# Kernel tuning notes

Hardware: AMD Instinct MI355X
Metric: run time of the kernel (lower is better)

Reference implementation:

```python
import jax, jax.numpy as jnp
import numpy as np

DIM = 2048
N_HEADS = 32
N_KV_HEADS = 8
HEAD_DIM = DIM // N_HEADS  # 64
GROUP = N_HEADS // N_KV_HEADS  # 4
ROPE_BASE = 10000.0


def setup_inputs() -> dict:
    key = jax.random.key(0)
    k1, k2, k3, k4, k5 = jax.random.split(key, 5)
    b, s = 1, 2048
    scale = 1.0 / np.sqrt(DIM)
    return {
        "x": jax.random.normal(k1, (b, s, DIM), dtype=jnp.float32),
        # weights stored as (in, out); equivalent math to torch Linear (x @ W.T)
        "wq": jax.random.normal(k2, (DIM, N_HEADS * HEAD_DIM), dtype=jnp.float32) * scale,
        "wk": jax.random.normal(k3, (DIM, N_KV_HEADS * HEAD_DIM), dtype=jnp.float32) * scale,
        "wv": jax.random.normal(k4, (DIM, N_KV_HEADS * HEAD_DIM), dtype=jnp.float32) * scale,
        "wo": jax.random.normal(k5, (N_HEADS * HEAD_DIM, DIM), dtype=jnp.float32) * scale,
    }


def _rope_cos_sin(seq_len, dtype):
    inv_freq = 1.0 / (ROPE_BASE ** (jnp.arange(0, HEAD_DIM, 2, dtype=jnp.float32) / HEAD_DIM))
    t = jnp.arange(seq_len, dtype=jnp.float32)
    freqs = jnp.outer(t, inv_freq)              # [s, hd/2]
    emb = jnp.concatenate([freqs, freqs], -1)   # [s, hd]
    return jnp.cos(emb).astype(dtype), jnp.sin(emb).astype(dtype)


def _rotate_half(x):
    x1, x2 = x[..., : HEAD_DIM // 2], x[..., HEAD_DIM // 2 :]
    return jnp.concatenate([-x2, x1], axis=-1)


def reference(x, wq, wk, wv, wo):
    b, s, _ = x.shape
    q = (x @ wq).reshape(b, s, N_HEADS, HEAD_DIM)
    k = (x @ wk).reshape(b, s, N_KV_HEADS, HEAD_DIM)
    v = (x @ wv).reshape(b, s, N_KV_HEADS, HEAD_DIM)

    cos, sin = _rope_cos_sin(s, x.dtype)
    cos = cos[None, :, None, :]  # [1, s, 1, hd] broadcast over batch & heads
    sin = sin[None, :, None, :]
    q = q * cos + _rotate_half(q) * sin
    k = k * cos + _rotate_half(k) * sin

    # GQA: repeat KV heads (repeat_interleave along head dim)
    k = jnp.repeat(k, GROUP, axis=2)  # [b, s, n_heads, hd]
    v = jnp.repeat(v, GROUP, axis=2)

    q = q.transpose(0, 2, 1, 3)  # [b, h, s, d]
    k = k.transpose(0, 2, 1, 3)
    v = v.transpose(0, 2, 1, 3)

    scores = jnp.einsum("bhqd,bhkd->bhqk", q, k) / jnp.sqrt(jnp.asarray(HEAD_DIM, x.dtype))
    attn = jax.nn.softmax(scores, axis=-1)
    out = jnp.einsum("bhqk,bhkd->bhqd", attn, v)
    out = out.transpose(0, 2, 1, 3).reshape(b, s, N_HEADS * HEAD_DIM)
    return out @ wo
```

## Files before the change

kernel.cpp:

```cpp
#include <hip/hip_runtime.h>
#include <hip/hip_bf16.h>

typedef __bf16 bf16x8 __attribute__((ext_vector_type(8)));
typedef __bf16 bf16x4 __attribute__((ext_vector_type(4)));
typedef float fx4 __attribute__((ext_vector_type(4)));
typedef float fx16 __attribute__((ext_vector_type(16)));

#define AS1 __attribute__((address_space(1)))
#define AS3 __attribute__((address_space(3)))

__global__ __launch_bounds__(256) void cast_x(const float4* __restrict__ X, __bf16* __restrict__ Xb) {
    int i = blockIdx.x * 256 + threadIdx.x;
    float4 v = X[i];
    bf16x4 o = { (__bf16)v.x, (__bf16)v.y, (__bf16)v.z, (__bf16)v.w };
    *(bf16x4*)(Xb + (size_t)i * 4) = o;
}

__global__ __launch_bounds__(256) void transpose_all(const float* __restrict__ wq, const float* __restrict__ wk,
                                                     const float* __restrict__ wv, const float* __restrict__ wo,
                                                     __bf16* __restrict__ WqkvT, __bf16* __restrict__ WoT) {
    constexpr int K = 2048;
    __shared__ float t[32][33];
    const int bx = blockIdx.x;
    const float* W; __bf16* Wt; int N, n0;
    if (bx < 64)      { W = wq; Wt = WqkvT;                        N = 2048; n0 = bx * 32; }
    else if (bx < 80) { W = wk; Wt = WqkvT + (size_t)2048 * 2048;  N = 512;  n0 = (bx - 64) * 32; }
    else if (bx < 96) { W = wv; Wt = WqkvT + (size_t)2560 * 2048;  N = 512;  n0 = (bx - 80) * 32; }
    else              { W = wo; Wt = WoT;                          N = 2048; n0 = (bx - 96) * 32; }
    const int tx = threadIdx.x & 31, ty = threadIdx.x >> 5;
    const int k0 = blockIdx.y * 32;
#pragma unroll
    for (int i = 0; i < 4; ++i)
        t[ty + i * 8][tx] = W[(size_t)(k0 + ty + i * 8) * N + n0 + tx];
    __syncthreads();
#pragma unroll
    for (int i = 0; i < 4; ++i)
        Wt[(size_t)(n0 + ty + i * 8) * K + k0 + tx] = (__bf16)t[tx][ty + i * 8];
}

__global__ __launch_bounds__(256) void gemm_qkv(const __bf16* __restrict__ A, const __bf16* __restrict__ Bt,
                                                __bf16* __restrict__ Qr, __bf16* __restrict__ Kr,
                                                __bf16* __restrict__ Vt) {
    constexpr int K = 2048;
    __shared__ __align__(16) __bf16 lA[2][128 * 32];
    __shared__ __align__(16) __bf16 lB[2][64 * 32];
    const int tid = threadIdx.x;
    const int wave = tid >> 6, lane = tid & 63;
    const int quad = lane >> 4, l16 = lane & 15;
    const int m0 = blockIdx.x * 128, n0 = blockIdx.y * 64;
    fx4 acc[2][4] = {};

    const __bf16* csrc[6]; __bf16* cdst[6];
#pragma unroll
    for (int it = 0; it < 6; ++it) {
        const int idx = wave * 6 + it;
        const int r4 = lane >> 2, c8 = (lane & 3) * 8;
        if (idx < 16) {
            const int kh = idx & 1, s = idx >> 1;
            csrc[it] = A + (size_t)(m0 + s * 16 + r4) * K + kh * 32 + c8;
            cdst[it] = &lA[kh][s * 512 + lane * 8];
        } else {
            const int b = idx - 16, kh = b & 1, s = b >> 1;
            csrc[it] = Bt + (size_t)(n0 + s * 16 + r4) * K + kh * 32 + c8;
            cdst[it] = &lB[kh][s * 512 + lane * 8];
        }
    }

    for (int k0 = 0; k0 < K; k0 += 64) {
        __syncthreads();
#pragma unroll
        for (int it = 0; it < 6; ++it)
            __builtin_amdgcn_global_load_lds((const AS1 void*)(csrc[it] + k0),
                                             (AS3 void*)cdst[it], 16, 0, 0);
        __builtin_amdgcn_s_waitcnt(0);
        __syncthreads();

#pragma unroll
        for (int kc = 0; kc < 2; ++kc) {
            bf16x8 af[2], bfr[4];
#pragma unroll
            for (int i = 0; i < 2; ++i) af[i] = *(const bf16x8*)&lA[kc][(wave * 32 + i * 16 + l16) * 32 + quad * 8];
#pragma unroll
            for (int j = 0; j < 4; ++j) bfr[j] = *(const bf16x8*)&lB[kc][(j * 16 + l16) * 32 + quad * 8];
#pragma unroll
            for (int i = 0; i < 2; ++i)
#pragma unroll
                for (int j = 0; j < 4; ++j)
                    acc[i][j] = __builtin_amdgcn_mfma_f32_16x16x32_bf16(af[i], bfr[j], acc[i][j], 0, 0, 0);
        }
    }

    const int by = blockIdx.y;
    if (by < 40) {
        const float scale = (by < 32) ? 0.18033688011112042f : 1.0f;
        __bf16* base = (by < 32) ? (Qr + (size_t)by * 2048 * 64)
                                 : (Kr + (size_t)(by - 32) * 2048 * 64);
#pragma unroll
        for (int jj = 0; jj < 2; ++jj) {
            const int dlo = jj * 16 + l16;
            const float inv = __builtin_amdgcn_exp2f(-(float)dlo * 0.41524101186092029f);
#pragma unroll
            for (int i = 0; i < 2; ++i)
#pragma unroll
                for (int r = 0; r < 4; ++r) {
                    const int s = m0 + wave * 32 + i * 16 + quad * 4 + r;
                    float sn, cs;
                    __sincosf((float)s * inv, &sn, &cs);
                    const float lo = acc[i][jj][r], hv = acc[i][jj + 2][r];
                    base[(size_t)s * 64 + dlo]      = (__bf16)((lo * cs - hv * sn) * scale);
                    base[(size_t)s * 64 + dlo + 32] = (__bf16)((hv * cs + lo * sn) * scale);
                }
        }
    } else {
        __bf16* vb = Vt + (size_t)(by - 40) * 64 * 2048;
#pragma unroll
        for (int i = 0; i < 2; ++i)
#pragma unroll
            for (int j = 0; j < 4; ++j) {
                const int d = j * 16 + l16;
                const int s0 = m0 + wave * 32 + i * 16 + quad * 4;
                bf16x4 p;
#pragma unroll
                for (int r = 0; r < 4; ++r) p[r] = (__bf16)acc[i][j][r];
                *(bf16x4*)&vb[(size_t)d * 2048 + s0] = p;
            }
    }
}

__global__ __launch_bounds__(256) void gemm_bt_sk(const __bf16* __restrict__ A, const __bf16* __restrict__ Bt,
                                                  float* __restrict__ C0, float* __restrict__ C1,
                                                  int M, int N, int K) {
    __shared__ __align__(16) __bf16 lA[128 * 32];
    __shared__ __align__(16) __bf16 lB[128 * 32];
    const int tid = threadIdx.x;
    const int wave = tid >> 6, lane = tid & 63;
    const int quad = lane >> 4, l16 = lane & 15;
    const int m0 = blockIdx.x * 128, n0 = blockIdx.y * 128;
    const int kz = blockIdx.z;
    const int kbeg = kz * (K >> 1), kend = kbeg + (K >> 1);
    float* C = kz ? C1 : C0;
    const int wm = (wave >> 1) * 64, wn = (wave & 1) * 64;
    fx4 acc[4][4] = {};

    const int st0 = wave * 1024;
    const int st1 = 4096 + wave * 1024;
    const int r0 = (st0 + lane * 16) >> 6, c0 = ((st0 + lane * 16) & 63) >> 1;
    const int r1 = (st1 + lane * 16) >> 6, c1 = ((st1 + lane * 16) & 63) >> 1;

    for (int k0 = kbeg; k0 < kend; k0 += 32) {
        __syncthreads();
        __builtin_amdgcn_global_load_lds((const AS1 void*)(A + (size_t)(m0 + r0) * K + k0 + c0),
                                         (AS3 void*)(lA + (st0 >> 1)), 16, 0, 0);
        __builtin_amdgcn_global_load_lds((const AS1 void*)(A + (size_t)(m0 + r1) * K + k0 + c1),
                                         (AS3 void*)(lA + (st1 >> 1)), 16, 0, 0);
        __builtin_amdgcn_global_load_lds((const AS1 void*)(Bt + (size_t)(n0 + r0) * K + k0 + c0),
                                         (AS3 void*)(lB + (st0 >> 1)), 16, 0, 0);
        __builtin_amdgcn_global_load_lds((const AS1 void*)(Bt + (size_t)(n0 + r1) * K + k0 + c1),
                                         (AS3 void*)(lB + (st1 >> 1)), 16, 0, 0);
        __builtin_amdgcn_s_waitcnt(0);
        __syncthreads();

        bf16x8 af[4], bfr[4];
#pragma unroll
        for (int i = 0; i < 4; ++i) af[i] = *(const bf16x8*)&lA[(wm + i * 16 + l16) * 32 + quad * 8];
#pragma unroll
        for (int j = 0; j < 4; ++j) bfr[j] = *(const bf16x8*)&lB[(wn + j * 16 + l16) * 32 + quad * 8];
#pragma unroll
        for (int i = 0; i < 4; ++i)
#pragma unroll
            for (int j = 0; j < 4; ++j)
                acc[i][j] = __builtin_amdgcn_mfma_f32_16x16x32_bf16(af[i], bfr[j], acc[i][j], 0, 0, 0);
    }
#pragma unroll
    for (int i = 0; i < 4; ++i)
#pragma unroll
        for (int j = 0; j < 4; ++j) {
            const int row = m0 + wm + i * 16 + quad * 4;
            const int col = n0 + wn + j * 16 + l16;
#pragma unroll
            for (int r = 0; r < 4; ++r)
                C[(size_t)(row + r) * N + col] = acc[i][j][r];
        }
}

__global__ __launch_bounds__(256) void reduce_add(float4* __restrict__ out, const float4* __restrict__ p) {
    const int i = blockIdx.x * 256 + threadIdx.x;
    float4 a = out[i];
    const float4 b = p[i];
    a.x += b.x; a.y += b.y; a.z += b.z; a.w += b.w;
    out[i] = a;
}

__global__ __launch_bounds__(512, 4) void flash_attn(const __bf16* __restrict__ Qr, const __bf16* __restrict__ Kr,
                                                     const __bf16* __restrict__ Vt, __bf16* __restrict__ O) {
    constexpr int S = 2048;
    __shared__ __align__(16) __bf16 smem[2][4 * 64 * 72];
    const int qt = blockIdx.x, h = blockIdx.y, kvh = h >> 2;
    const int tid = threadIdx.x, wave = tid >> 6, lane = tid & 63;
    const int grp = wave >> 2, w4 = wave & 3;
    const int l32 = lane & 31, hi = lane >> 5;
    const int goff = grp * 2 * 4608;

    const int qrow = qt * 128 + w4 * 32 + l32;
    const __bf16* qptr = Qr + ((size_t)h * S + qrow) * 64;
    bf16x8 qf[4];
#pragma unroll
    for (int kc = 0; kc < 4; ++kc) qf[kc] = *(const bf16x8*)(qptr + kc * 16 + hi * 8);

    const __bf16* Kbase = Kr + (size_t)kvh * S * 64;
    const __bf16* Vbase = Vt + (size_t)kvh * 64 * S;

    const int gtid = tid & 255;
    const int krow = gtid >> 3;
    const int kcol = (gtid & 7) * 8;
    const int vslot = (kcol & 48) | ((kcol & 8) >> 1);

    bf16x8 kreg0 = *(const bf16x8*)(Kbase + (size_t)(grp * 64 + krow) * 64 + kcol);
    bf16x8 kreg1 = *(const bf16x8*)(Kbase + (size_t)(grp * 64 + 32 + krow) * 64 + kcol);
    bf16x8 vreg0 = *(const bf16x8*)(Vbase + (size_t)krow * S + grp * 64 + kcol);
    bf16x8 vreg1 = *(const bf16x8*)(Vbase + (size_t)(32 + krow) * S + grp * 64 + kcol);

    fx16 ov0, ov1;
#pragma unroll
    for (int i = 0; i < 16; ++i) { ov0[i] = 0.f; ov1[i] = 0.f; }
    float l_acc = 0.f;

    {
        __bf16* nK = &smem[0][goff];
        __bf16* nV = nK + 4608;
        *(bf16x8*)&nK[krow * 72 + kcol] = kreg0;
        *(bf16x8*)&nK[(32 + krow) * 72 + kcol] = kreg1;
        bf16x4 v0lo = { vreg0[0], vreg0[1], vreg0[2], vreg0[3] };
        bf16x4 v0hi = { vreg0[4], vreg0[5], vreg0[6], vreg0[7] };
        bf16x4 v1lo = { vreg1[0], vreg1[1], vreg1[2], vreg1[3] };
        bf16x4 v1hi = { vreg1[4], vreg1[5], vreg1[6], vreg1[7] };
        *(bf16x4*)&nV[krow * 72 + vslot]            = v0lo;
        *(bf16x4*)&nV[krow * 72 + vslot + 8]        = v0hi;
        *(bf16x4*)&nV[(32 + krow) * 72 + vslot]     = v1lo;
        *(bf16x4*)&nV[(32 + krow) * 72 + vslot + 8] = v1hi;
        const int kt1 = 2 + grp;
        kreg0 = *(const bf16x8*)(Kbase + (size_t)(kt1 * 64 + krow) * 64 + kcol);
        kreg1 = *(const bf16x8*)(Kbase + (size_t)(kt1 * 64 + 32 + krow) * 64 + kcol);
        vreg0 = *(const bf16x8*)(Vbase + (size_t)krow * S + kt1 * 64 + kcol);
        vreg1 = *(const bf16x8*)(Vbase + (size_t)(32 + krow) * S + kt1 * 64 + kcol);
    }
    __syncthreads();

    for (int it = 0; it < 16; ++it) {
        __bf16* lKg = &smem[it & 1][goff];
        __bf16* lVg = lKg + 4608;

        if (it + 1 < 16) {
            __bf16* nK = &smem[(it + 1) & 1][goff];
            __bf16* nV = nK + 4608;
            *(bf16x8*)&nK[krow * 72 + kcol] = kreg0;
            *(bf16x8*)&nK[(32 + krow) * 72 + kcol] = kreg1;
            bf16x4 v0lo = { vreg0[0], vreg0[1], vreg0[2], vreg0[3] };
            bf16x4 v0hi = { vreg0[4], vreg0[5], vreg0[6], vreg0[7] };
            bf16x4 v1lo = { vreg1[0], vreg1[1], vreg1[2], vreg1[3] };
            bf16x4 v1hi = { vreg1[4], vreg1[5], vreg1[6], vreg1[7] };
            *(bf16x4*)&nV[krow * 72 + vslot]            = v0lo;
            *(bf16x4*)&nV[krow * 72 + vslot + 8]        = v0hi;
            *(bf16x4*)&nV[(32 + krow) * 72 + vslot]     = v1lo;
            *(bf16x4*)&nV[(32 + krow) * 72 + vslot + 8] = v1hi;
            const int it2 = (it + 2 < 16) ? it + 2 : 15;
            const int ktn = it2 * 2 + grp;
            kreg0 = *(const bf16x8*)(Kbase + (size_t)(ktn * 64 + krow) * 64 + kcol);
            kreg1 = *(const bf16x8*)(Kbase + (size_t)(ktn * 64 + 32 + krow) * 64 + kcol);
            vreg0 = *(const bf16x8*)(Vbase + (size_t)krow * S + ktn * 64 + kcol);
            vreg1 = *(const bf16x8*)(Vbase + (size_t)(32 + krow) * S + ktn * 64 + kcol);
        }

        fx16 sc0, sc1;
#pragma unroll
        for (int i = 0; i < 16; ++i) { sc0[i] = 0.f; sc1[i] = 0.f; }
#pragma unroll
        for (int kc = 0; kc < 4; ++kc) {
            const bf16x8 a0 = *(const bf16x8*)&lKg[l32 * 72 + kc * 16 + hi * 8];
            const bf16x8 a1 = *(const bf16x8*)&lKg[(32 + l32) * 72 + kc * 16 + hi * 8];
            sc0 = __builtin_amdgcn_mfma_f32_32x32x16_bf16(a0, qf[kc], sc0, 0, 0, 0);
            sc1 = __builtin_amdgcn_mfma_f32_32x32x16_bf16(a1, qf[kc], sc1, 0, 0, 0);
        }

#pragma unroll
        for (int h2 = 0; h2 < 2; ++h2) {
#pragma unroll
            for (int c = 0; c < 2; ++c) {
                bf16x8 pb;
#pragma unroll
                for (int j = 0; j < 8; ++j) {
                    const float sv = h2 ? sc1[c * 8 + j] : sc0[c * 8 + j];
                    const float p = __builtin_amdgcn_exp2f(sv);
                    l_acc += p;
                    pb[j] = (__bf16)p;
                }
                const int kcv = h2 * 2 + c;
                const bf16x8 va0 = *(const bf16x8*)&lVg[l32 * 72 + kcv * 16 + hi * 8];
                const bf16x8 va1 = *(const bf16x8*)&lVg[(32 + l32) * 72 + kcv * 16 + hi * 8];
                ov0 = __builtin_amdgcn_mfma_f32_32x32x16_bf16(va0, pb, ov0, 0, 0, 0);
                ov1 = __builtin_amdgcn_mfma_f32_32x32x16_bf16(va1, pb, ov1, 0, 0, 0);
            }
        }
        __syncthreads();
    }

    const float l_pair = l_acc + __shfl_xor(l_acc, 32, 64);

    fx4* lO = (fx4*)&smem[0][0];
    float* lL = (float*)(&smem[0][0] + 16384);
    if (grp == 1) {
#pragma unroll
        for (int ic = 0; ic < 4; ++ic) {
            fx4 c0, c1;
#pragma unroll
            for (int r = 0; r < 4; ++r) { c0[r] = ov0[ic * 4 + r]; c1[r] = ov1[ic * 4 + r]; }
            lO[(ic * 4 + w4) * 64 + lane] = c0;
            lO[((ic + 4) * 4 + w4) * 64 + lane] = c1;
        }
        if (hi == 0) lL[w4 * 32 + l32] = l_pair;
    }
    __syncthreads();
    if (grp == 0) {
#pragma unroll
        for (int ic = 0; ic < 4; ++ic) {
            const fx4 c0 = lO[(ic * 4 + w4) * 64 + lane];
            const fx4 c1 = lO[((ic + 4) * 4 + w4) * 64 + lane];
#pragma unroll
            for (int r = 0; r < 4; ++r) { ov0[ic * 4 + r] += c0[r]; ov1[ic * 4 + r] += c1[r]; }
        }
        const float inv_l = 1.0f / (l_pair + lL[w4 * 32 + l32]);
#pragma unroll
        for (int dt = 0; dt < 2; ++dt)
#pragma unroll
            for (int rg2 = 0; rg2 < 4; ++rg2) {
                bf16x4 o4;
#pragma unroll
                for (int r = 0; r < 4; ++r)
                    o4[r] = (__bf16)((dt ? ov1[rg2 * 4 + r] : ov0[rg2 * 4 + r]) * inv_l);
                const int col = h * 64 + dt * 32 + rg2 * 8 + hi * 4;
                *(bf16x4*)(O + (size_t)qrow * 2048 + col) = o4;
            }
    }
}

extern "C" void kernel_launch(void* const* d_in, const int* in_sizes, int n_in,
                              void* d_out, int out_size, void* d_ws, size_t ws_size,
                              hipStream_t stream) {
    const float* x  = (const float*)d_in[0];
    const float* wq = (const float*)d_in[1];
    const float* wk = (const float*)d_in[2];
    const float* wv = (const float*)d_in[3];
    const float* wo = (const float*)d_in[4];
    float* out = (float*)d_out;
    char* ws = (char*)d_ws;

    __bf16* Xb    = (__bf16*)ws;
    __bf16* WqkvT = (__bf16*)(ws + ((size_t)8 << 20));
    __bf16* WoT   = (__bf16*)(ws + ((size_t)20 << 20));
    __bf16* Qr    = (__bf16*)(ws + ((size_t)28 << 20));
    __bf16* Kr    = (__bf16*)(ws + ((size_t)36 << 20));
    __bf16* Vt    = (__bf16*)(ws + ((size_t)38 << 20));
    __bf16* Ob    = (__bf16*)(ws + ((size_t)40 << 20));
    float*  Cp    = (float*)ws;

    cast_x<<<4096, 256, 0, stream>>>((const float4*)x, Xb);
    transpose_all<<<dim3(160, 64), 256, 0, stream>>>(wq, wk, wv, wo, WqkvT, WoT);

    gemm_qkv<<<dim3(16, 48), 256, 0, stream>>>(Xb, WqkvT, Qr, Kr, Vt);
    flash_attn<<<dim3(16, 32), 512, 0, stream>>>(Qr, Kr, Vt, Ob);
    gemm_bt_sk<<<dim3(16, 16, 2), 256, 0, stream>>>(Ob, WoT, out, Cp, 2048, 2048, 2048);
    reduce_add<<<4096, 256, 0, stream>>>((float4*)out, (const float4*)Cp);
}
```

Baseline: 222.1 us.

## Fuse prep kernels and double-buffer GEMM loads with XOR-swizzled LDS

Merges the x cast and the weight transpose into one launch, with larger transpose tiles and paired bf16 stores. Both GEMMs now use a double-buffered LDS pipeline that prefetches the next K-slice while MFMAs run on the current one, cutting the barrier count. LDS column offsets are XOR-swizzled to reduce bank conflicts. The cost is more LDS per block and more complex indexing.

```diff
diff --git a/kernel.cpp b/kernel.cpp
--- a/kernel.cpp
+++ b/kernel.cpp
@@ -3,91 +3,105 @@
 
 typedef __bf16 bf16x8 __attribute__((ext_vector_type(8)));
 typedef __bf16 bf16x4 __attribute__((ext_vector_type(4)));
+typedef __bf16 bf16x2 __attribute__((ext_vector_type(2)));
 typedef float fx4 __attribute__((ext_vector_type(4)));
 typedef float fx16 __attribute__((ext_vector_type(16)));
 
 #define AS1 __attribute__((address_space(1)))
 #define AS3 __attribute__((address_space(3)))
 
-__global__ __launch_bounds__(256) void cast_x(const float4* __restrict__ X, __bf16* __restrict__ Xb) {
-    int i = blockIdx.x * 256 + threadIdx.x;
-    float4 v = X[i];
-    bf16x4 o = { (__bf16)v.x, (__bf16)v.y, (__bf16)v.z, (__bf16)v.w };
-    *(bf16x4*)(Xb + (size_t)i * 4) = o;
-}
-
-__global__ __launch_bounds__(256) void transpose_all(const float* __restrict__ wq, const float* __restrict__ wk,
-                                                     const float* __restrict__ wv, const float* __restrict__ wo,
-                                                     __bf16* __restrict__ WqkvT, __bf16* __restrict__ WoT) {
+__global__ __launch_bounds__(256) void prep(const float4* __restrict__ X, __bf16* __restrict__ Xb,
+                                            const float* __restrict__ wq, const float* __restrict__ wk,
+                                            const float* __restrict__ wv, const float* __restrict__ wo,
+                                            __bf16* __restrict__ WqkvT, __bf16* __restrict__ WoT) {
+    const int bx = blockIdx.x;
+    if (bx < 4096) {
+        const int i = bx * 256 + threadIdx.x;
+        const float4 v = X[i];
+        bf16x4 o = { (__bf16)v.x, (__bf16)v.y, (__bf16)v.z, (__bf16)v.w };
+        *(bf16x4*)(Xb + (size_t)i * 4) = o;
+        return;
+    }
     constexpr int K = 2048;
-    __shared__ float t[32][33];
-    const int bx = blockIdx.x;
-    const float* W; __bf16* Wt; int N, n0;
-    if (bx < 64)      { W = wq; Wt = WqkvT;                        N = 2048; n0 = bx * 32; }
-    else if (bx < 80) { W = wk; Wt = WqkvT + (size_t)2048 * 2048;  N = 512;  n0 = (bx - 64) * 32; }
-    else if (bx < 96) { W = wv; Wt = WqkvT + (size_t)2560 * 2048;  N = 512;  n0 = (bx - 80) * 32; }
-    else              { W = wo; Wt = WoT;                          N = 2048; n0 = (bx - 96) * 32; }
+    __shared__ float t[64][33];
+    const int tt = bx - 4096;
+    const float* W; __bf16* Wt; int N, loc;
+    if (tt < 2048)      { W = wq; Wt = WqkvT;                       N = 2048; loc = tt; }
+    else if (tt < 2560) { W = wk; Wt = WqkvT + (size_t)2048 * 2048; N = 512;  loc = tt - 2048; }
+    else if (tt < 3072) { W = wv; Wt = WqkvT + (size_t)2560 * 2048; N = 512;  loc = tt - 2560; }
+    else                { W = wo; Wt = WoT;                         N = 2048; loc = tt - 3072; }
+    const int k0 = (loc & 31) * 64, n0 = (loc >> 5) * 32;
     const int tx = threadIdx.x & 31, ty = threadIdx.x >> 5;
-    const int k0 = blockIdx.y * 32;
-#pragma unroll
-    for (int i = 0; i < 4; ++i)
+#pragma unroll
+    for (int i = 0; i < 8; ++i)
         t[ty + i * 8][tx] = W[(size_t)(k0 + ty + i * 8) * N + n0 + tx];
     __syncthreads();
 #pragma unroll
-    for (int i = 0; i < 4; ++i)
-        Wt[(size_t)(n0 + ty + i * 8) * K + k0 + tx] = (__bf16)t[tx][ty + i * 8];
+    for (int i = 0; i < 4; ++i) {
+        const int nn = ty + i * 8;
+        bf16x2 o = { (__bf16)t[tx * 2][nn], (__bf16)t[tx * 2 + 1][nn] };
+        *(bf16x2*)&Wt[(size_t)(n0 + nn) * K + k0 + tx * 2] = o;
+    }
 }
 
 __global__ __launch_bounds__(256) void gemm_qkv(const __bf16* __restrict__ A, const __bf16* __restrict__ Bt,
                                                 __bf16* __restrict__ Qr, __bf16* __restrict__ Kr,
                                                 __bf16* __restrict__ Vt) {
     constexpr int K = 2048;
-    __shared__ __align__(16) __bf16 lA[2][128 * 32];
-    __shared__ __align__(16) __bf16 lB[2][64 * 32];
+    constexpr int BUF = 192 * 32;
+    __shared__ __align__(16) __bf16 sm[2][BUF];
     const int tid = threadIdx.x;
     const int wave = tid >> 6, lane = tid & 63;
     const int quad = lane >> 4, l16 = lane & 15;
     const int m0 = blockIdx.x * 128, n0 = blockIdx.y * 64;
     fx4 acc[2][4] = {};
 
-    const __bf16* csrc[6]; __bf16* cdst[6];
-#pragma unroll
-    for (int it = 0; it < 6; ++it) {
-        const int idx = wave * 6 + it;
-        const int r4 = lane >> 2, c8 = (lane & 3) * 8;
-        if (idx < 16) {
-            const int kh = idx & 1, s = idx >> 1;
-            csrc[it] = A + (size_t)(m0 + s * 16 + r4) * K + kh * 32 + c8;
-            cdst[it] = &lA[kh][s * 512 + lane * 8];
+    const int r4 = lane >> 2;
+    const int c8s = ((lane & 3) ^ ((r4 >> 1) & 3)) * 8;
+    const __bf16* csrc[3]; int cdst[3];
+#pragma unroll
+    for (int it = 0; it < 3; ++it) {
+        const int idx = wave * 3 + it;
+        if (idx < 8) {
+            csrc[it] = A + (size_t)(m0 + idx * 16 + r4) * K + c8s;
+            cdst[it] = idx * 512 + lane * 8;
         } else {
-            const int b = idx - 16, kh = b & 1, s = b >> 1;
-            csrc[it] = Bt + (size_t)(n0 + s * 16 + r4) * K + kh * 32 + c8;
-            cdst[it] = &lB[kh][s * 512 + lane * 8];
-        }
-    }
-
-    for (int k0 = 0; k0 < K; k0 += 64) {
-        __syncthreads();
-#pragma unroll
-        for (int it = 0; it < 6; ++it)
-            __builtin_amdgcn_global_load_lds((const AS1 void*)(csrc[it] + k0),
-                                             (AS3 void*)cdst[it], 16, 0, 0);
-        __builtin_amdgcn_s_waitcnt(0);
-        __syncthreads();
-
-#pragma unroll
-        for (int kc = 0; kc < 2; ++kc) {
-            bf16x8 af[2], bfr[4];
-#pragma unroll
-            for (int i = 0; i < 2; ++i) af[i] = *(const bf16x8*)&lA[kc][(wave * 32 + i * 16 + l16) * 32 + quad * 8];
-#pragma unroll
-            for (int j = 0; j < 4; ++j) bfr[j] = *(const bf16x8*)&lB[kc][(j * 16 + l16) * 32 + quad * 8];
-#pragma unroll
-            for (int i = 0; i < 2; ++i)
-#pragma unroll
-                for (int j = 0; j < 4; ++j)
-                    acc[i][j] = __builtin_amdgcn_mfma_f32_16x16x32_bf16(af[i], bfr[j], acc[i][j], 0, 0, 0);
-        }
+            const int s = idx - 8;
+            csrc[it] = Bt + (size_t)(n0 + s * 16 + r4) * K + c8s;
+            cdst[it] = 4096 + s * 512 + lane * 8;
+        }
+    }
+    const int colr = (quad ^ ((l16 >> 1) & 3)) * 8;
+    const int arow = (wave * 32 + l16) * 32 + colr;
+    const int brow = 4096 + l16 * 32 + colr;
+
+#pragma unroll
+    for (int it = 0; it < 3; ++it)
+        __builtin_amdgcn_global_load_lds((const AS1 void*)csrc[it], (AS3 void*)&sm[0][cdst[it]], 16, 0, 0);
+    __builtin_amdgcn_s_waitcnt(0);
+    __syncthreads();
+
+#pragma unroll 2
+    for (int t = 0; t < 64; ++t) {
+        if (t < 63) {
+            const int kofs = (t + 1) * 32;
+#pragma unroll
+            for (int it = 0; it < 3; ++it)
+                __builtin_amdgcn_global_load_lds((const AS1 void*)(csrc[it] + kofs),
+                                                 (AS3 void*)&sm[(t + 1) & 1][cdst[it]], 16, 0, 0);
+        }
+        const __bf16* cb = sm[t & 1];
+        bf16x8 af[2], bfr[4];
+#pragma unroll
+        for (int i = 0; i < 2; ++i) af[i] = *(const bf16x8*)&cb[arow + i * 512];
+#pragma unroll
+        for (int j = 0; j < 4; ++j) bfr[j] = *(const bf16x8*)&cb[brow + j * 512];
+#pragma unroll
+        for (int i = 0; i < 2; ++i)
+#pragma unroll
+            for (int j = 0; j < 4; ++j)
+                acc[i][j] = __builtin_amdgcn_mfma_f32_16x16x32_bf16(af[i], bfr[j], acc[i][j], 0, 0, 0);
+        if (t < 63) { __builtin_amdgcn_s_waitcnt(0); __syncthreads(); }
     }
 
     const int by = blockIdx.y;
@@ -129,47 +143,66 @@
 
 __global__ __launch_bounds__(256) void gemm_bt_sk(const __bf16* __restrict__ A, const __bf16* __restrict__ Bt,
                                                   float* __restrict__ C0, float* __restrict__ C1,
-                                                  int M, int N, int K) {
-    __shared__ __align__(16) __bf16 lA[128 * 32];
-    __shared__ __align__(16) __bf16 lB[128 * 32];
+                                                  int M, int N, int Kdim) {
+    constexpr int K = 2048;
+    constexpr int BUF = 256 * 32;
+    __shared__ __align__(16) __bf16 sm[2][BUF];
     const int tid = threadIdx.x;
     const int wave = tid >> 6, lane = tid & 63;
     const int quad = lane >> 4, l16 = lane & 15;
     const int m0 = blockIdx.x * 128, n0 = blockIdx.y * 128;
     const int kz = blockIdx.z;
-    const int kbeg = kz * (K >> 1), kend = kbeg + (K >> 1);
     float* C = kz ? C1 : C0;
     const int wm = (wave >> 1) * 64, wn = (wave & 1) * 64;
     fx4 acc[4][4] = {};
 
-    const int st0 = wave * 1024;
-    const int st1 = 4096 + wave * 1024;
-    const int r0 = (st0 + lane * 16) >> 6, c0 = ((st0 + lane * 16) & 63) >> 1;
-    const int r1 = (st1 + lane * 16) >> 6, c1 = ((st1 + lane * 16) & 63) >> 1;
-
-    for (int k0 = kbeg; k0 < kend; k0 += 32) {
-        __syncthreads();
-        __builtin_amdgcn_global_load_lds((const AS1 void*)(A + (size_t)(m0 + r0) * K + k0 + c0),
-                                         (AS3 void*)(lA + (st0 >> 1)), 16, 0, 0);
-        __builtin_amdgcn_global_load_lds((const AS1 void*)(A + (size_t)(m0 + r1) * K + k0 + c1),
-                                         (AS3 void*)(lA + (st1 >> 1)), 16, 0, 0);
-        __builtin_amdgcn_global_load_lds((const AS1 void*)(Bt + (size_t)(n0 + r0) * K + k0 + c0),
-                                         (AS3 void*)(lB + (st0 >> 1)), 16, 0, 0);
-        __builtin_amdgcn_global_load_lds((const AS1 void*)(Bt + (size_t)(n0 + r1) * K + k0 + c1),
-                                         (AS3 void*)(lB + (st1 >> 1)), 16, 0, 0);
-        __builtin_amdgcn_s_waitcnt(0);
-        __syncthreads();
-
+    const int r4 = lane >> 2;
+    const int c8s = ((lane & 3) ^ ((r4 >> 1) & 3)) * 8;
+    const __bf16* csrc[4]; int cdst[4];
+#pragma unroll
+    for (int it = 0; it < 4; ++it) {
+        const int idx = wave * 4 + it;
+        if (idx < 8) {
+            csrc[it] = A + (size_t)(m0 + idx * 16 + r4) * K + c8s;
+            cdst[it] = idx * 512 + lane * 8;
+        } else {
+            const int s = idx - 8;
+            csrc[it] = Bt + (size_t)(n0 + s * 16 + r4) * K + c8s;
+            cdst[it] = 4096 + s * 512 + lane * 8;
+        }
+    }
+    const int colr = (quad ^ ((l16 >> 1) & 3)) * 8;
+    const int arow = (wm + l16) * 32 + colr;
+    const int brow = 4096 + (wn + l16) * 32 + colr;
+
+    const int kbeg = kz * 1024;
+#pragma unroll
+    for (int it = 0; it < 4; ++it)
+        __builtin_amdgcn_global_load_lds((const AS1 void*)(csrc[it] + kbeg), (AS3 void*)&sm[0][cdst[it]], 16, 0, 0);
+    __builtin_amdgcn_s_waitcnt(0);
+    __syncthreads();
+
+#pragma unroll 2
+    for (int t = 0; t < 32; ++t) {
+        if (t < 31) {
+            const int kofs = kbeg + (t + 1) * 32;
+#pragma unroll
+            for (int it = 0; it < 4; ++it)
+                __builtin_amdgcn_global_load_lds((const AS1 void*)(csrc[it] + kofs),
+                                                 (AS3 void*)&sm[(t + 1) & 1][cdst[it]], 16, 0, 0);
+        }
+        const __bf16* cb = sm[t & 1];
         bf16x8 af[4], bfr[4];
 #pragma unroll
-        for (int i = 0; i < 4; ++i) af[i] = *(const bf16x8*)&lA[(wm + i * 16 + l16) * 32 + quad * 8];
-#pragma unroll
-        for (int j = 0; j < 4; ++j) bfr[j] = *(const bf16x8*)&lB[(wn + j * 16 + l16) * 32 + quad * 8];
+        for (int i = 0; i < 4; ++i) af[i] = *(const bf16x8*)&cb[arow + i * 512];
+#pragma unroll
+        for (int j = 0; j < 4; ++j) bfr[j] = *(const bf16x8*)&cb[brow + j * 512];
 #pragma unroll
         for (int i = 0; i < 4; ++i)
 #pragma unroll
             for (int j = 0; j < 4; ++j)
                 acc[i][j] = __builtin_amdgcn_mfma_f32_16x16x32_bf16(af[i], bfr[j], acc[i][j], 0, 0, 0);
+        if (t < 31) { __builtin_amdgcn_s_waitcnt(0); __syncthreads(); }
     }
 #pragma unroll
     for (int i = 0; i < 4; ++i)
@@ -363,9 +396,7 @@
     __bf16* Ob    = (__bf16*)(ws + ((size_t)40 << 20));
     float*  Cp    = (float*)ws;
 
-    cast_x<<<4096, 256, 0, stream>>>((const float4*)x, Xb);
-    transpose_all<<<dim3(160, 64), 256, 0, stream>>>(wq, wk, wv, wo, WqkvT, WoT);
-
+    prep<<<4096 + 5120, 256, 0, stream>>>((const float4*)x, Xb, wq, wk, wv, wo, WqkvT, WoT);
     gemm_qkv<<<dim3(16, 48), 256, 0, stream>>>(Xb, WqkvT, Qr, Kr, Vt);
     flash_attn<<<dim3(16, 32), 512, 0, stream>>>(Qr, Kr, Vt, Ob);
     gemm_bt_sk<<<dim3(16, 16, 2), 256, 0, stream>>>(Ob, WoT, out, Cp, 2048, 2048, 2048);
```

Result: faster. 214.6 us (-3.4%).
